# Kernel tuning notes

Measured on AMD Instinct MI355X. Metric: run time of the kernel, lower is better.

## Reference

```python
import jax, jax.numpy as jnp
import numpy as np

B, S, D, N = 16, 1024, 512, 2048
SPECTRAL_RADIUS = 0.95
SPARSITY = 0.01  # effective_sparsity = max(0.01, 5/N) = 0.01 for N=2048


def setup_inputs() -> dict:
    key = jax.random.key(0)
    k_x, k_fb, k_wraw, k_mask, k_win, k_wfb = jax.random.split(key, 6)
    x_seq = jax.random.normal(k_x, (B, S, D), dtype=jnp.float32)
    feedback_seq = jax.random.normal(k_fb, (B, S, D), dtype=jnp.float32)
    initial_state = jnp.zeros((B, N), dtype=jnp.float32)
    # Fixed random reservoir: sparse gaussian rescaled to spectral radius ~0.95.
    # For an NxN gaussian with density p, spectral radius ~= sqrt(N*p), so we
    # rescale by SPECTRAL_RADIUS / sqrt(N*p) (the torch code uses the exact
    # max eigenvalue; this approximation preserves the same math structure).
    W_raw = jax.random.normal(k_wraw, (N, N), dtype=jnp.float32)
    mask = (jax.random.uniform(k_mask, (N, N)) < SPARSITY).astype(jnp.float32)
    W_res = W_raw * mask * (SPECTRAL_RADIUS / jnp.sqrt(N * SPARSITY))
    W_in = jax.random.normal(k_win, (N, D), dtype=jnp.float32) * 0.1
    W_fb = jax.random.normal(k_wfb, (N, D), dtype=jnp.float32) * 0.1
    return {
        "x_seq": x_seq,
        "feedback_seq": feedback_seq,
        "initial_state": initial_state,
        "W_res": W_res,
        "W_in": W_in,
        "W_fb": W_fb,
    }


def reference(x_seq, feedback_seq, initial_state, W_res, W_in, W_fb):
    # Precompute input + feedback projections as one batched GEMM each
    # (same math as per-step einsums: 'bi,ni->bn' == x @ W.T).
    drive = jnp.einsum("bsd,nd->sbn", x_seq, W_in) + jnp.einsum(
        "bsd,nd->sbn", feedback_seq, W_fb
    )  # (S, B, N)

    def step(state, drive_t):
        # pre = state @ W_res.T + W_in x_t + W_fb fb_t
        new_state = jnp.tanh(state @ W_res.T + drive_t)
        return new_state, new_state

    _, states = jax.lax.scan(step, initial_state, drive)  # (S, B, N)
    return jnp.transpose(states, (1, 0, 2))  # (B, S, N)
```

## Files before the change

### kernel.cpp

```cpp
#include <hip/hip_runtime.h>
#include <stdint.h>

typedef unsigned short u16;
typedef unsigned int   u32;
typedef __attribute__((ext_vector_type(8))) short short8;
typedef __attribute__((ext_vector_type(4))) float f32x4;

#define CAP   52

__device__ __forceinline__ u16 rne_bf16(float f){
  u32 u = __float_as_uint(f);
  u32 r = (u + 0x7fffu + ((u >> 16) & 1u)) >> 16;
  return (u16)r;
}
__device__ __forceinline__ float bf16_to_f(u16 h){
  return __uint_as_float(((u32)h) << 16);
}
__device__ __forceinline__ float tanh_fast(float x){
  float e = __expf(2.0f * x);
  return 1.0f - 2.0f / (e + 1.0f);
}

__global__ __launch_bounds__(256) void pack_a_k(const float* __restrict__ x,
                                                const float* __restrict__ fb,
                                                u16* __restrict__ A){
  int idx = blockIdx.x * 256 + threadIdx.x;
  int m = idx >> 9, d = idx & 511;
  float xv = x[idx];
  float fv = fb[idx];
  u16 xh = rne_bf16(xv); u16 xl = rne_bf16(xv - bf16_to_f(xh));
  u16 fh = rne_bf16(fv); u16 fl = rne_bf16(fv - bf16_to_f(fh));
  size_t base = (size_t)m * 2048;
  A[base + d]        = xh;
  A[base + 512 + d]  = fh;
  A[base + 1024 + d] = xl;
  A[base + 1536 + d] = fl;
}

__global__ __launch_bounds__(256) void pack_b_k(const float* __restrict__ Win,
                                                const float* __restrict__ Wfb,
                                                const int* __restrict__ rowperm,
                                                u16* __restrict__ Bm){
  int idx = blockIdx.x * 256 + threadIdx.x;
  int n = idx >> 9, d = idx & 511;
  int row = rowperm[n];
  float iv = Win[(size_t)row * 512 + d];
  float fv = Wfb[(size_t)row * 512 + d];
  u16 ih = rne_bf16(iv); u16 il = rne_bf16(iv - bf16_to_f(ih));
  u16 fh = rne_bf16(fv); u16 fl = rne_bf16(fv - bf16_to_f(fh));
  size_t base = (size_t)n * 3072;
  Bm[base + d]        = ih;
  Bm[base + 512 + d]  = fh;
  Bm[base + 1024 + d] = ih;
  Bm[base + 1536 + d] = fh;
  Bm[base + 2048 + d] = il;
  Bm[base + 2560 + d] = fl;
}

#define GLDS(gp, lp) __builtin_amdgcn_global_load_lds( \
    (const __attribute__((address_space(1))) void*)(gp), \
    (__attribute__((address_space(3))) void*)(lp), 16, 0, 0)

__global__ __launch_bounds__(256) void gemm_k(const u16* __restrict__ A,
                                              const u16* __restrict__ Bm,
                                              float* __restrict__ C){
  __shared__ __align__(16) u16 As[128 * 32];
  __shared__ __align__(16) u16 Bs[128 * 32];
  const int tid = threadIdx.x;
  const int w = tid >> 6, l = tid & 63;
  const int bid = blockIdx.x;
  const int mt = bid >> 4, nt = bid & 15;
  const int m0 = mt * 128, n0 = nt * 128;
  const int srow = tid >> 2;
  const int scol = (tid & 3) * 8;
  const int wr = w & 1, wc = w >> 1;
  const int lhi = l >> 4, llo = l & 15;

  f32x4 acc[4][4];
  #pragma unroll
  for (int i = 0; i < 4; i++)
    #pragma unroll
    for (int j = 0; j < 4; j++)
      acc[i][j] = (f32x4){0.f, 0.f, 0.f, 0.f};

  for (int kt = 0; kt < 96; ++kt){
    int k = kt * 32;
    int keff = (k >= 2048) ? (k - 2048) : k;
    #pragma unroll
    for (int r = 0; r < 2; r++){
      const u16* ga = A  + (size_t)(m0 + r * 64 + srow) * 2048 + keff + scol;
      GLDS(ga, &As[r * 2048 + w * 512]);
      const u16* gb = Bm + (size_t)(n0 + r * 64 + srow) * 3072 + k + scol;
      GLDS(gb, &Bs[r * 2048 + w * 512]);
    }
    __syncthreads();
    short8 af[4], bf[4];
    #pragma unroll
    for (int i = 0; i < 4; i++){
      af[i] = *(const short8*)&As[(wr * 64 + i * 16 + llo) * 32 + lhi * 8];
      bf[i] = *(const short8*)&Bs[(wc * 64 + i * 16 + llo) * 32 + lhi * 8];
    }
    #pragma unroll
    for (int i = 0; i < 4; i++)
      #pragma unroll
      for (int j = 0; j < 4; j++)
        acc[i][j] = __builtin_amdgcn_mfma_f32_16x16x32_bf16(af[i], bf[j], acc[i][j], 0, 0, 0);
    __syncthreads();
  }
  #pragma unroll
  for (int i = 0; i < 4; i++)
    #pragma unroll
    for (int j = 0; j < 4; j++)
      #pragma unroll
      for (int rg = 0; rg < 4; rg++){
        int mr = m0 + wr * 64 + i * 16 + lhi * 4 + rg;
        int nc = n0 + wc * 64 + j * 16 + llo;
        C[(size_t)mr * 2048 + nc] = acc[i][j][rg];
      }
}

__global__ __launch_bounds__(256) void count_k(const float* __restrict__ W,
                                               int* __restrict__ nnz){
  int gt = blockIdx.x * 256 + threadIdx.x;
  int row = gt >> 6, l = gt & 63;
  const float* wr = W + (size_t)row * 2048;
  int c = 0;
  for (int i = 0; i < 32; i++) c += (wr[i * 64 + l] != 0.0f) ? 1 : 0;
  for (int off = 32; off; off >>= 1) c += __shfl_down(c, off, 64);
  if (l == 0) nnz[row] = c;
}

__global__ __launch_bounds__(1024) void sort_k(const int* __restrict__ nnz,
                                               u32* __restrict__ rowsp,
                                               int* __restrict__ L1a,
                                               int* __restrict__ rowperm){
  __shared__ int hist[64], off[64], cur[64];
  __shared__ int order[2048];
  int tid = threadIdx.x;
  if (tid < 64){ hist[tid] = 0; cur[tid] = 0; }
  __syncthreads();
  for (int r = tid; r < 2048; r += 1024){
    int b = nnz[r]; if (b > 63) b = 63;
    atomicAdd(&hist[b], 1);
  }
  __syncthreads();
  if (tid == 0){
    int run = 0;
    for (int b = 63; b >= 0; b--){ off[b] = run; run += hist[b]; }
  }
  __syncthreads();
  for (int r = tid; r < 2048; r += 1024){
    int b = nnz[r]; if (b > 63) b = 63;
    int pos = off[b] + atomicAdd(&cur[b], 1);
    order[pos] = r;
  }
  __syncthreads();
  int rA = order[tid], rB = order[2047 - tid];
  rowsp[tid] = (u32)rA | ((u32)rB << 16);
  L1a[tid] = nnz[rA];
  rowperm[tid] = rA;
  rowperm[tid + 1024] = rB;
}

__global__ __launch_bounds__(256) void fill_k(const float* __restrict__ W,
                                              const u32* __restrict__ rowsp,
                                              u32* __restrict__ wpk){
  int gt = blockIdx.x * 256 + threadIdx.x;
  int p = gt >> 6, l = gt & 63;
  u32 rp = rowsp[p];
  int rA = (int)(rp & 0xffffu), rB = (int)(rp >> 16);
  int base = 0;
  for (int h = 0; h < 2; h++){
    int row = h ? rB : rA;
    const float* wr = W + (size_t)row * 2048;
    int cnt = 0;
    for (int i = 0; i < 32; i++){
      int c = i * 64 + l;
      float v = wr[c];
      unsigned long long m = __ballot(v != 0.0f);
      int pre = __popcll(m & ((1ull << l) - 1ull));
      if (v != 0.0f){
        int s = base + cnt + pre;
        if (s < CAP){
          u32 addr = (u32)c << 2;
          u32 u = __float_as_uint(v);
          u = ((u - addr + 0x1000u) & 0xFFFFE000u) + addr;
          wpk[s * 1024 + p] = u;
        }
      }
      cnt += __popcll(m);
    }
    base += cnt;
  }
  for (int s = base + l; s < CAP; s += 64)
    wpk[s * 1024 + p] = 0u;
}

__global__ __launch_bounds__(64) void sched_k(u32* wpk,
                                              const u32* __restrict__ rowsp,
                                              const int* __restrict__ nnz){
  __shared__ u32 itm[64 * CAP];
  __shared__ int cnt[32];
  const int lane = threadIdx.x;
  const int p = blockIdx.x * 64 + lane;
  u32 rp = rowsp[p];
  int rA = (int)(rp & 0xffffu), rB = (int)(rp >> 16);
  int L1 = nnz[rA]; if (L1 > CAP) L1 = CAP;
  int nT = L1 + nnz[rB]; if (nT > CAP) nT = CAP;
  for (int k = 0; k < CAP; k++) itm[lane * CAP + k] = wpk[k * 1024 + p];
  __syncthreads();
  unsigned long long used = 0ull;
  for (int s = 0; s < CAP; s++){
    if (lane < 32) cnt[lane] = 0;
    __syncthreads();
    u32 word;
    if (s < nT){
      int lo = (s < L1) ? 0 : L1;
      int hi = (s < L1) ? L1 : nT;
      int chosen = -1;
      for (int capc = 2; chosen < 0; capc++){
        for (int j = lo; j < hi; j++){
          if (used & (1ull << j)) continue;
          u32 w = itm[lane * CAP + j];
          int bk = (int)((w >> 2) & 31u);
          int old = atomicAdd(&cnt[bk], 1);
          if (old < capc){ chosen = j; break; }
          atomicSub(&cnt[bk], 1);
        }
      }
      used |= 1ull << chosen;
      word = itm[lane * CAP + chosen];
    } else {
      int bsel = -1;
      for (int capc = 2; bsel < 0; capc++){
        for (int bk = 0; bk < 32; bk++){
          int old = atomicAdd(&cnt[bk], 1);
          if (old < capc){ bsel = bk; break; }
          atomicSub(&cnt[bk], 1);
        }
      }
      word = (u32)bsel << 2;
    }
    __syncthreads();
    wpk[s * 1024 + p] = word;
  }
}

__global__ __attribute__((amdgpu_flat_work_group_size(1024, 1024),
                          amdgpu_waves_per_eu(4, 4)))
void rnn_k(float* __restrict__ out,
           const float* __restrict__ init,
           const u32* __restrict__ wpkg,
           const u32* __restrict__ rowsp,
           const int* __restrict__ L1a){
  const int tid = threadIdx.x, b = blockIdx.x;
  u32 wk[CAP];
  #pragma unroll
  for (int k = 0; k < CAP; k++) wk[k] = wpkg[k * 1024 + tid];
  u32 rp = rowsp[tid];
  int rA = (int)(rp & 0xffffu), rB = (int)(rp >> 16);
  int L1 = L1a[tid];

  __shared__ float st[2048];
  st[tid]        = init[(size_t)b * 2048 + tid];
  st[tid + 1024] = init[(size_t)b * 2048 + tid + 1024];
  __syncthreads();
  const char* stb = (const char*)st;

  float* ob = out + (size_t)b * 1024 * 2048;
  float dA = __builtin_nontemporal_load(&ob[tid]);
  float dB = __builtin_nontemporal_load(&ob[tid + 1024]);
  for (int t = 0; t < 1024; t++){
    float* orow = ob + (size_t)t * 2048;
    const float* nrow = ob + (size_t)((t + 1) & 1023) * 2048;
    float dA2 = __builtin_nontemporal_load(&nrow[tid]);
    float dB2 = __builtin_nontemporal_load(&nrow[tid + 1024]);
    float aAll = 0.f, aA = 0.f;
    #pragma unroll
    for (int k = 0; k < CAP; k++){
      u32 w = wk[k];
      float sv = *(const float*)(stb + (w & 0x1FFCu));
      float pv = __uint_as_float(w) * sv;
      aAll += pv;
      aA += (k < L1) ? pv : 0.0f;
    }
    float preA = aA + dA;
    float preB = (aAll - aA) + dB;
    __syncthreads();
    float sA = tanh_fast(preA);
    float sB = tanh_fast(preB);
    st[rA] = sA; st[rB] = sB;
    __syncthreads();
    __builtin_nontemporal_store(st[tid], &orow[tid]);
    __builtin_nontemporal_store(st[tid + 1024], &orow[tid + 1024]);
    dA = dA2; dB = dB2;
  }
}

extern "C" void kernel_launch(void* const* d_in, const int* in_sizes, int n_in,
                              void* d_out, int out_size, void* d_ws, size_t ws_size,
                              hipStream_t stream) {
  const float* x    = (const float*)d_in[0];
  const float* fb   = (const float*)d_in[1];
  const float* init = (const float*)d_in[2];
  const float* Wres = (const float*)d_in[3];
  const float* Win  = (const float*)d_in[4];
  const float* Wfb  = (const float*)d_in[5];
  float* out = (float*)d_out;

  char* w8 = (char*)d_ws;
  u16*  A_pack = (u16*)(w8);
  u16*  B_pack = (u16*)(w8 + 67108864);
  u32*  wpk    = (u32*) (w8 + 79691776);
  int*  nnz    = (int*) (w8 + 79904768);
  u32*  rowsp  = (u32*) (w8 + 79912960);
  int*  L1a    = (int*) (w8 + 79917056);
  int*  rowperm= (int*) (w8 + 79921152);

  pack_a_k<<<32768, 256, 0, stream>>>(x, fb, A_pack);
  count_k<<<512, 256, 0, stream>>>(Wres, nnz);
  sort_k<<<1, 1024, 0, stream>>>(nnz, rowsp, L1a, rowperm);
  pack_b_k<<<4096, 256, 0, stream>>>(Win, Wfb, rowperm, B_pack);
  fill_k<<<256, 256, 0, stream>>>(Wres, rowsp, wpk);
  sched_k<<<16, 64, 0, stream>>>(wpk, rowsp, nnz);
  gemm_k<<<2048, 256, 0, stream>>>(A_pack, B_pack, out);
  rnn_k<<<16, 1024, 0, stream>>>(out, init, wpk, rowsp, L1a);
}
```

Baseline: 3.162 ms.

## Add iterative swap sweeps to reduce LDS bank conflicts in reservoir weight schedule

```diff
diff --git a/kernel.cpp b/kernel.cpp
--- a/kernel.cpp
+++ b/kernel.cpp
@@ -7,6 +7,7 @@
 typedef __attribute__((ext_vector_type(4))) float f32x4;
 
 #define CAP   52
+#define NSWEEP 48
 
 __device__ __forceinline__ u16 rne_bf16(float f){
   u32 u = __float_as_uint(f);
@@ -199,20 +200,23 @@
 __global__ __launch_bounds__(64) void sched_k(u32* wpk,
                                               const u32* __restrict__ rowsp,
                                               const int* __restrict__ nnz){
-  __shared__ u32 itm[64 * CAP];
-  __shared__ int cnt[32];
+  __shared__ u32 pool[CAP * 64];
+  __shared__ u32 itm[CAP * 64];
+  __shared__ int cnt[CAP * 32];
   const int lane = threadIdx.x;
   const int p = blockIdx.x * 64 + lane;
   u32 rp = rowsp[p];
   int rA = (int)(rp & 0xffffu), rB = (int)(rp >> 16);
   int L1 = nnz[rA]; if (L1 > CAP) L1 = CAP;
   int nT = L1 + nnz[rB]; if (nT > CAP) nT = CAP;
-  for (int k = 0; k < CAP; k++) itm[lane * CAP + k] = wpk[k * 1024 + p];
-  __syncthreads();
+
+  for (int i = lane; i < CAP * 32; i += 64) cnt[i] = 0;
+  for (int k = 0; k < CAP; k++) pool[k * 64 + lane] = wpk[k * 1024 + p];
+  __builtin_amdgcn_s_waitcnt(0);
+
   unsigned long long used = 0ull;
   for (int s = 0; s < CAP; s++){
-    if (lane < 32) cnt[lane] = 0;
-    __syncthreads();
+    int* c = &cnt[s * 32];
     u32 word;
     if (s < nT){
       int lo = (s < L1) ? 0 : L1;
@@ -221,29 +225,85 @@
       for (int capc = 2; chosen < 0; capc++){
         for (int j = lo; j < hi; j++){
           if (used & (1ull << j)) continue;
-          u32 w = itm[lane * CAP + j];
+          u32 w = pool[j * 64 + lane];
           int bk = (int)((w >> 2) & 31u);
-          int old = atomicAdd(&cnt[bk], 1);
+          int old = atomicAdd(&c[bk], 1);
           if (old < capc){ chosen = j; break; }
-          atomicSub(&cnt[bk], 1);
+          atomicSub(&c[bk], 1);
         }
       }
       used |= 1ull << chosen;
-      word = itm[lane * CAP + chosen];
+      word = pool[chosen * 64 + lane];
     } else {
       int bsel = -1;
       for (int capc = 2; bsel < 0; capc++){
-        for (int bk = 0; bk < 32; bk++){
-          int old = atomicAdd(&cnt[bk], 1);
+        for (int bk0 = 0; bk0 < 32; bk0++){
+          int bk = (bk0 + lane) & 31;
+          int old = atomicAdd(&c[bk], 1);
           if (old < capc){ bsel = bk; break; }
-          atomicSub(&cnt[bk], 1);
+          atomicSub(&c[bk], 1);
         }
       }
       word = (u32)bsel << 2;
     }
-    __syncthreads();
-    wpk[s * 1024 + p] = word;
-  }
+    itm[s * 64 + lane] = word;
+  }
+
+  for (int sweep = 0; sweep < NSWEEP; sweep++){
+    int fixes = 0;
+    for (int s1 = 0; s1 < CAP; s1++){
+      u32 w1 = itm[s1 * 64 + lane];
+      int b1 = (int)((w1 >> 2) & 31u);
+      if (cnt[s1 * 32 + b1] <= 2) continue;
+      if (s1 >= nT){
+        for (int bk0 = 1; bk0 < 32; bk0++){
+          int b2 = (b1 + bk0 + lane) & 31;
+          int old = atomicAdd(&cnt[s1 * 32 + b2], 1);
+          if (old < 2){
+            atomicSub(&cnt[s1 * 32 + b1], 1);
+            itm[s1 * 64 + lane] = (u32)b2 << 2;
+            fixes++; break;
+          }
+          atomicSub(&cnt[s1 * 32 + b2], 1);
+        }
+        continue;
+      }
+      int lo = (s1 < L1) ? 0 : L1;
+      int hi = (s1 < L1) ? L1 : nT;
+      int len = hi - lo;
+      if (len < 2) continue;
+      for (int d = 1; d < len; d++){
+        int s2 = lo + ((s1 - lo) + d + lane + sweep * 7) % len;
+        if (s2 == s1) continue;
+        u32 w2 = itm[s2 * 64 + lane];
+        int b2 = (int)((w2 >> 2) & 31u);
+        if (b1 == b2) continue;
+        if (cnt[s2 * 32 + b1] >= 2) continue;
+        if (cnt[s1 * 32 + b2] >= 2) continue;
+        int a = atomicSub(&cnt[s1 * 32 + b1], 1);
+        if (a <= 2){ atomicAdd(&cnt[s1 * 32 + b1], 1); break; }
+        int c2 = atomicAdd(&cnt[s1 * 32 + b2], 1);
+        if (c2 >= 2){
+          atomicSub(&cnt[s1 * 32 + b2], 1);
+          atomicAdd(&cnt[s1 * 32 + b1], 1); continue;
+        }
+        int c3 = atomicAdd(&cnt[s2 * 32 + b1], 1);
+        if (c3 >= 2){
+          atomicSub(&cnt[s2 * 32 + b1], 1);
+          atomicSub(&cnt[s1 * 32 + b2], 1);
+          atomicAdd(&cnt[s1 * 32 + b1], 1); continue;
+        }
+        atomicSub(&cnt[s2 * 32 + b2], 1);
+        itm[s1 * 64 + lane] = w2;
+        itm[s2 * 64 + lane] = w1;
+        fixes++; break;
+      }
+    }
+    if (__ballot(fixes != 0) == 0ull) break;
+  }
+
+  for (int s = 0; s < CAP; s++)
+    wpk[s * 1024 + p] = itm[s * 64 + lane];
 }
 
 __global__ __attribute__((amdgpu_flat_work_group_size(1024, 1024),
```

Result: slower. 3.985 ms (+26.0%).

## Double-buffer reservoir state and duplicate rotated copies to cut barriers and bank conflicts

Applied to the files above, without the earlier changes.

```diff
diff --git a/kernel.cpp b/kernel.cpp
--- a/kernel.cpp
+++ b/kernel.cpp
@@ -7,6 +7,7 @@
 typedef __attribute__((ext_vector_type(4))) float f32x4;
 
 #define CAP   52
+#define ROT   7
 
 __device__ __forceinline__ u16 rne_bf16(float f){
   u32 u = __float_as_uint(f);
@@ -164,7 +165,7 @@
 
 __global__ __launch_bounds__(256) void fill_k(const float* __restrict__ W,
                                               const u32* __restrict__ rowsp,
-                                              u32* __restrict__ wpk){
+                                              u32* __restrict__ raw){
   int gt = blockIdx.x * 256 + threadIdx.x;
   int p = gt >> 6, l = gt & 63;
   u32 rp = rowsp[p];
@@ -182,24 +183,22 @@
       if (v != 0.0f){
         int s = base + cnt + pre;
         if (s < CAP){
-          u32 addr = (u32)c << 2;
           u32 u = __float_as_uint(v);
-          u = ((u - addr + 0x1000u) & 0xFFFFE000u) + addr;
-          wpk[s * 1024 + p] = u;
+          u = ((u + 0x1000u) & 0xFFFFE000u) | (u32)c;
+          raw[s * 1024 + p] = u;
         }
       }
       cnt += __popcll(m);
     }
     base += cnt;
   }
-  for (int s = base + l; s < CAP; s += 64)
-    wpk[s * 1024 + p] = 0u;
-}
-
-__global__ __launch_bounds__(64) void sched_k(u32* wpk,
+}
+
+__global__ __launch_bounds__(64) void sched_k(const u32* __restrict__ raw,
+                                              u32* __restrict__ wpk,
                                               const u32* __restrict__ rowsp,
                                               const int* __restrict__ nnz){
-  __shared__ u32 itm[64 * CAP];
+  __shared__ u32 pool[CAP * 64];
   __shared__ int cnt[32];
   const int lane = threadIdx.x;
   const int p = blockIdx.x * 64 + lane;
@@ -207,12 +206,15 @@
   int rA = (int)(rp & 0xffffu), rB = (int)(rp >> 16);
   int L1 = nnz[rA]; if (L1 > CAP) L1 = CAP;
   int nT = L1 + nnz[rB]; if (nT > CAP) nT = CAP;
-  for (int k = 0; k < CAP; k++) itm[lane * CAP + k] = wpk[k * 1024 + p];
-  __syncthreads();
+
+  for (int k = 0; k < CAP; k++) pool[k * 64 + lane] = raw[k * 1024 + p];
+  __syncthreads();
+
   unsigned long long used = 0ull;
   for (int s = 0; s < CAP; s++){
     if (lane < 32) cnt[lane] = 0;
     __syncthreads();
+    const int par = s & 1;
     u32 word;
     if (s < nT){
       int lo = (s < L1) ? 0 : L1;
@@ -221,19 +223,24 @@
       for (int capc = 2; chosen < 0; capc++){
         for (int j = lo; j < hi; j++){
           if (used & (1ull << j)) continue;
-          u32 w = itm[lane * CAP + j];
-          int bk = (int)((w >> 2) & 31u);
+          int c = (int)(pool[j * 64 + lane] & 0x7FFu);
+          int bk = (par ? (c + ROT) : c) & 31;
           int old = atomicAdd(&cnt[bk], 1);
           if (old < capc){ chosen = j; break; }
           atomicSub(&cnt[bk], 1);
         }
       }
       used |= 1ull << chosen;
-      word = itm[lane * CAP + chosen];
+      u32 r = pool[chosen * 64 + lane];
+      u32 vb = r & 0xFFFFE000u;
+      u32 c  = r & 0x7FFu;
+      u32 ad = (u32)((par ? ((c + ROT) & 2047) : (int)c) << 2);
+      word = ((vb - ad + 0x1000u) & 0xFFFFE000u) + ad;
     } else {
       int bsel = -1;
       for (int capc = 2; bsel < 0; capc++){
-        for (int bk = 0; bk < 32; bk++){
+        for (int bb = 0; bb < 32; bb++){
+          int bk = (bb + lane) & 31;
           int old = atomicAdd(&cnt[bk], 1);
           if (old < capc){ bsel = bk; break; }
           atomicSub(&cnt[bk], 1);
@@ -258,43 +265,62 @@
   #pragma unroll
   for (int k = 0; k < CAP; k++) wk[k] = wpkg[k * 1024 + tid];
   u32 rp = rowsp[tid];
-  int rA = (int)(rp & 0xffffu), rB = (int)(rp >> 16);
-  int L1 = L1a[tid];
-
-  __shared__ float st[2048];
-  st[tid]        = init[(size_t)b * 2048 + tid];
-  st[tid + 1024] = init[(size_t)b * 2048 + tid + 1024];
+  const int rA = (int)(rp & 0xffffu), rB = (int)(rp >> 16);
+  const int L1 = L1a[tid];
+  const int wA0 = rA << 2;
+  const int wA1 = (((rA + ROT) & 2047) << 2) + 8192;
+  const int wB0 = rB << 2;
+  const int wB1 = (((rB + ROT) & 2047) << 2) + 8192;
+
+  __shared__ float st[8192];
+  float i0 = init[(size_t)b * 2048 + tid];
+  float i1 = init[(size_t)b * 2048 + tid + 1024];
+  st[tid] = i0;
+  st[tid + 1024] = i1;
+  st[2048 + ((tid + ROT) & 2047)] = i0;
+  st[2048 + ((tid + 1024 + ROT) & 2047)] = i1;
   __syncthreads();
   const char* stb = (const char*)st;
+  char* stw = (char*)st;
+  const int t4a = tid << 2, t4b = (tid + 1024) << 2;
 
   float* ob = out + (size_t)b * 1024 * 2048;
   float dA = __builtin_nontemporal_load(&ob[tid]);
   float dB = __builtin_nontemporal_load(&ob[tid + 1024]);
-  for (int t = 0; t < 1024; t++){
-    float* orow = ob + (size_t)t * 2048;
-    const float* nrow = ob + (size_t)((t + 1) & 1023) * 2048;
-    float dA2 = __builtin_nontemporal_load(&nrow[tid]);
-    float dB2 = __builtin_nontemporal_load(&nrow[tid + 1024]);
-    float aAll = 0.f, aA = 0.f;
-    #pragma unroll
-    for (int k = 0; k < CAP; k++){
-      u32 w = wk[k];
-      float sv = *(const float*)(stb + (w & 0x1FFCu));
-      float pv = __uint_as_float(w) * sv;
-      aAll += pv;
-      aA += (k < L1) ? pv : 0.0f;
-    }
-    float preA = aA + dA;
-    float preB = (aAll - aA) + dB;
-    __syncthreads();
-    float sA = tanh_fast(preA);
-    float sB = tanh_fast(preB);
-    st[rA] = sA; st[rB] = sB;
-    __syncthreads();
-    __builtin_nontemporal_store(st[tid], &orow[tid]);
-    __builtin_nontemporal_store(st[tid + 1024], &orow[tid + 1024]);
-    dA = dA2; dB = dB2;
-  }
+
+#define ESN_STEP(T, RD, WR) { \
+    float* orow = ob + (size_t)(T) * 2048; \
+    const float* nrow = ob + (size_t)(((T) + 1) & 1023) * 2048; \
+    float dA2 = __builtin_nontemporal_load(&nrow[tid]); \
+    float dB2 = __builtin_nontemporal_load(&nrow[tid + 1024]); \
+    float aAll = 0.f, aA = 0.f; \
+    _Pragma("unroll") \
+    for (int k = 0; k < CAP; k++){ \
+      u32 w = wk[k]; \
+      float sv = *(const float*)(stb + (RD) + ((k & 1) ? 8192 : 0) + (w & 0x1FFCu)); \
+      float pv = __uint_as_float(w) * sv; \
+      aAll += pv; \
+      aA += (k < L1) ? pv : 0.0f; \
+    } \
+    float preA = aA + dA; \
+    float preB = (aAll - aA) + dB; \
+    float sA = tanh_fast(preA); \
+    float sB = tanh_fast(preB); \
+    *(float*)(stw + (WR) + wA0) = sA; \
+    *(float*)(stw + (WR) + wA1) = sA; \
+    *(float*)(stw + (WR) + wB0) = sB; \
+    *(float*)(stw + (WR) + wB1) = sB; \
+    __syncthreads(); \
+    __builtin_nontemporal_store(*(const float*)(stb + (WR) + t4a), &orow[tid]); \
+    __builtin_nontemporal_store(*(const float*)(stb + (WR) + t4b), &orow[tid + 1024]); \
+    dA = dA2; dB = dB2; \
+  }
+
+  for (int t = 0; t < 1024; t += 2){
+    ESN_STEP(t, 0, 16384)
+    ESN_STEP(t + 1, 16384, 0)
+  }
+#undef ESN_STEP
 }
 
 extern "C" void kernel_launch(void* const* d_in, const int* in_sizes, int n_in,
@@ -316,13 +342,14 @@
   u32*  rowsp  = (u32*) (w8 + 79912960);
   int*  L1a    = (int*) (w8 + 79917056);
   int*  rowperm= (int*) (w8 + 79921152);
+  u32*  raw    = (u32*) out;
 
   pack_a_k<<<32768, 256, 0, stream>>>(x, fb, A_pack);
   count_k<<<512, 256, 0, stream>>>(Wres, nnz);
   sort_k<<<1, 1024, 0, stream>>>(nnz, rowsp, L1a, rowperm);
   pack_b_k<<<4096, 256, 0, stream>>>(Win, Wfb, rowperm, B_pack);
-  fill_k<<<256, 256, 0, stream>>>(Wres, rowsp, wpk);
-  sched_k<<<16, 64, 0, stream>>>(wpk, rowsp, nnz);
+  fill_k<<<256, 256, 0, stream>>>(Wres, rowsp, raw);
+  sched_k<<<16, 64, 0, stream>>>(raw, wpk, rowsp, nnz);
   gemm_k<<<2048, 256, 0, stream>>>(A_pack, B_pack, out);
   rnn_k<<<16, 1024, 0, stream>>>(out, init, wpk, rowsp, L1a);
 }
```

After: 3.582 ms. +13.3%, slower.

## Split each batch recurrence across two workgroups with global flag handshake

Applied to the files above, without the earlier changes.

```diff
diff --git a/kernel.cpp b/kernel.cpp
--- a/kernel.cpp
+++ b/kernel.cpp
@@ -6,7 +6,7 @@
 typedef __attribute__((ext_vector_type(8))) short short8;
 typedef __attribute__((ext_vector_type(4))) float f32x4;
 
-#define CAP   52
+#define CAP   56
 
 __device__ __forceinline__ u16 rne_bf16(float f){
   u32 u = __float_as_uint(f);
@@ -133,38 +133,47 @@
 __global__ __launch_bounds__(1024) void sort_k(const int* __restrict__ nnz,
                                                u32* __restrict__ rowsp,
                                                int* __restrict__ L1a,
-                                               int* __restrict__ rowperm){
-  __shared__ int hist[64], off[64], cur[64];
+                                               int* __restrict__ rowperm,
+                                               int* __restrict__ flags){
+  __shared__ int hist[128], off[128], cur[128];
   __shared__ int order[2048];
   int tid = threadIdx.x;
-  if (tid < 64){ hist[tid] = 0; cur[tid] = 0; }
-  __syncthreads();
-  for (int r = tid; r < 2048; r += 1024){
-    int b = nnz[r]; if (b > 63) b = 63;
-    atomicAdd(&hist[b], 1);
-  }
-  __syncthreads();
-  if (tid == 0){
+  if (tid < 32) flags[tid] = 0;
+  if (tid < 128){ hist[tid] = 0; cur[tid] = 0; }
+  __syncthreads();
+  {
+    int b0 = nnz[tid]; if (b0 > 63) b0 = 63;
+    atomicAdd(&hist[b0], 1);
+    int b1 = nnz[tid + 1024]; if (b1 > 63) b1 = 63;
+    atomicAdd(&hist[64 + b1], 1);
+  }
+  __syncthreads();
+  if (tid < 2){
     int run = 0;
-    for (int b = 63; b >= 0; b--){ off[b] = run; run += hist[b]; }
-  }
-  __syncthreads();
-  for (int r = tid; r < 2048; r += 1024){
-    int b = nnz[r]; if (b > 63) b = 63;
-    int pos = off[b] + atomicAdd(&cur[b], 1);
-    order[pos] = r;
-  }
-  __syncthreads();
-  int rA = order[tid], rB = order[2047 - tid];
+    for (int b = 63; b >= 0; b--){ off[tid * 64 + b] = run; run += hist[tid * 64 + b]; }
+  }
+  __syncthreads();
+  {
+    int b0 = nnz[tid]; if (b0 > 63) b0 = 63;
+    int pos = off[b0] + atomicAdd(&cur[b0], 1);
+    order[pos] = tid;
+    int b1 = nnz[tid + 1024]; if (b1 > 63) b1 = 63;
+    int pos1 = off[64 + b1] + atomicAdd(&cur[64 + b1], 1);
+    order[1024 + pos1] = tid + 1024;
+  }
+  __syncthreads();
+  int hh = tid >> 9, ii = tid & 511;
+  int rA = order[hh * 1024 + ii];
+  int rB = order[hh * 1024 + 1023 - ii];
   rowsp[tid] = (u32)rA | ((u32)rB << 16);
   L1a[tid] = nnz[rA];
-  rowperm[tid] = rA;
-  rowperm[tid + 1024] = rB;
+  rowperm[hh * 1024 + ii] = rA;
+  rowperm[hh * 1024 + 512 + ii] = rB;
 }
 
 __global__ __launch_bounds__(256) void fill_k(const float* __restrict__ W,
                                               const u32* __restrict__ rowsp,
-                                              u32* __restrict__ wpk){
+                                              u32* __restrict__ raw){
   int gt = blockIdx.x * 256 + threadIdx.x;
   int p = gt >> 6, l = gt & 63;
   u32 rp = rowsp[p];
@@ -182,24 +191,22 @@
       if (v != 0.0f){
         int s = base + cnt + pre;
         if (s < CAP){
-          u32 addr = (u32)c << 2;
           u32 u = __float_as_uint(v);
-          u = ((u - addr + 0x1000u) & 0xFFFFE000u) + addr;
-          wpk[s * 1024 + p] = u;
+          u = ((u + 0x1000u) & 0xFFFFE000u) | (u32)c;
+          raw[s * 1024 + p] = u;
         }
       }
       cnt += __popcll(m);
     }
     base += cnt;
   }
-  for (int s = base + l; s < CAP; s += 64)
-    wpk[s * 1024 + p] = 0u;
-}
-
-__global__ __launch_bounds__(64) void sched_k(u32* wpk,
+}
+
+__global__ __launch_bounds__(64) void sched_k(const u32* __restrict__ raw,
+                                              u32* __restrict__ wpk,
                                               const u32* __restrict__ rowsp,
                                               const int* __restrict__ nnz){
-  __shared__ u32 itm[64 * CAP];
+  __shared__ u32 pool[CAP * 64];
   __shared__ int cnt[32];
   const int lane = threadIdx.x;
   const int p = blockIdx.x * 64 + lane;
@@ -207,7 +214,7 @@
   int rA = (int)(rp & 0xffffu), rB = (int)(rp >> 16);
   int L1 = nnz[rA]; if (L1 > CAP) L1 = CAP;
   int nT = L1 + nnz[rB]; if (nT > CAP) nT = CAP;
-  for (int k = 0; k < CAP; k++) itm[lane * CAP + k] = wpk[k * 1024 + p];
+  for (int k = 0; k < CAP; k++) pool[k * 64 + lane] = raw[k * 1024 + p];
   __syncthreads();
   unsigned long long used = 0ull;
   for (int s = 0; s < CAP; s++){
@@ -221,19 +228,22 @@
       for (int capc = 2; chosen < 0; capc++){
         for (int j = lo; j < hi; j++){
           if (used & (1ull << j)) continue;
-          u32 w = itm[lane * CAP + j];
-          int bk = (int)((w >> 2) & 31u);
+          int bk = (int)(pool[j * 64 + lane] & 31u);
           int old = atomicAdd(&cnt[bk], 1);
           if (old < capc){ chosen = j; break; }
           atomicSub(&cnt[bk], 1);
         }
       }
       used |= 1ull << chosen;
-      word = itm[lane * CAP + chosen];
+      u32 r = pool[chosen * 64 + lane];
+      u32 vb = r & 0xFFFFE000u;
+      u32 ad = (r & 0x7FFu) << 2;
+      word = ((vb - ad + 0x1000u) & 0xFFFFE000u) + ad;
     } else {
       int bsel = -1;
       for (int capc = 2; bsel < 0; capc++){
-        for (int bk = 0; bk < 32; bk++){
+        for (int bb = 0; bb < 32; bb++){
+          int bk = (bb + lane) & 31;
           int old = atomicAdd(&cnt[bk], 1);
           if (old < capc){ bsel = bk; break; }
           atomicSub(&cnt[bk], 1);
@@ -246,35 +256,44 @@
   }
 }
 
-__global__ __attribute__((amdgpu_flat_work_group_size(1024, 1024),
-                          amdgpu_waves_per_eu(4, 4)))
+__global__ __attribute__((amdgpu_flat_work_group_size(512, 512),
+                          amdgpu_waves_per_eu(2, 2)))
 void rnn_k(float* __restrict__ out,
            const float* __restrict__ init,
            const u32* __restrict__ wpkg,
            const u32* __restrict__ rowsp,
-           const int* __restrict__ L1a){
-  const int tid = threadIdx.x, b = blockIdx.x;
+           const int* __restrict__ L1a,
+           int* flags){
+  const int tid = threadIdx.x;
+  const int b = blockIdx.x & 15, h = blockIdx.x >> 4;
+  const int q = h * 512 + tid;
   u32 wk[CAP];
   #pragma unroll
-  for (int k = 0; k < CAP; k++) wk[k] = wpkg[k * 1024 + tid];
-  u32 rp = rowsp[tid];
-  int rA = (int)(rp & 0xffffu), rB = (int)(rp >> 16);
-  int L1 = L1a[tid];
+  for (int k = 0; k < CAP; k++) wk[k] = wpkg[k * 1024 + q];
+  u32 rp = rowsp[q];
+  const int rA = (int)(rp & 0xffffu), rB = (int)(rp >> 16);
+  const int L1 = L1a[q];
+  const int own0 = h << 10, peer0 = (1 - h) << 10;
 
   __shared__ float st[2048];
-  st[tid]        = init[(size_t)b * 2048 + tid];
-  st[tid + 1024] = init[(size_t)b * 2048 + tid + 1024];
+  #pragma unroll
+  for (int j = 0; j < 4; j++)
+    st[j * 512 + tid] = init[(size_t)b * 2048 + j * 512 + tid];
   __syncthreads();
   const char* stb = (const char*)st;
 
   float* ob = out + (size_t)b * 1024 * 2048;
-  float dA = __builtin_nontemporal_load(&ob[tid]);
-  float dB = __builtin_nontemporal_load(&ob[tid + 1024]);
+  int* myf = &flags[h * 16 + b];
+  int* pf  = &flags[(1 - h) * 16 + b];
+
+  float dA = __builtin_nontemporal_load(&ob[own0 + tid]);
+  float dB = __builtin_nontemporal_load(&ob[own0 + 512 + tid]);
+
   for (int t = 0; t < 1024; t++){
-    float* orow = ob + (size_t)t * 2048;
+    float* row = ob + (size_t)t * 2048;
     const float* nrow = ob + (size_t)((t + 1) & 1023) * 2048;
-    float dA2 = __builtin_nontemporal_load(&nrow[tid]);
-    float dB2 = __builtin_nontemporal_load(&nrow[tid + 1024]);
+    float dA2 = __builtin_nontemporal_load(&nrow[own0 + tid]);
+    float dB2 = __builtin_nontemporal_load(&nrow[own0 + 512 + tid]);
     float aAll = 0.f, aA = 0.f;
     #pragma unroll
     for (int k = 0; k < CAP; k++){
@@ -284,15 +303,24 @@
       aAll += pv;
       aA += (k < L1) ? pv : 0.0f;
     }
-    float preA = aA + dA;
-    float preB = (aAll - aA) + dB;
-    __syncthreads();
-    float sA = tanh_fast(preA);
-    float sB = tanh_fast(preB);
+    float sA = tanh_fast(aA + dA);
+    float sB = tanh_fast((aAll - aA) + dB);
+    __builtin_nontemporal_store(sA, &row[rA]);
+    __builtin_nontemporal_store(sB, &row[rB]);
+    __syncthreads();
     st[rA] = sA; st[rB] = sB;
-    __syncthreads();
-    __builtin_nontemporal_store(st[tid], &orow[tid]);
-    __builtin_nontemporal_store(st[tid + 1024], &orow[tid + 1024]);
+    asm volatile("s_waitcnt vmcnt(0)" ::: "memory");
+    if (tid == 0){
+      __hip_atomic_store(myf, t + 1, __ATOMIC_RELAXED, __HIP_MEMORY_SCOPE_AGENT);
+      while (__hip_atomic_load(pf, __ATOMIC_ACQUIRE, __HIP_MEMORY_SCOPE_AGENT) <= t)
+        __builtin_amdgcn_s_sleep(1);
+    }
+    __syncthreads();
+    float p0 = __builtin_nontemporal_load(&row[peer0 + tid]);
+    float p1 = __builtin_nontemporal_load(&row[peer0 + 512 + tid]);
+    st[peer0 + tid] = p0;
+    st[peer0 + 512 + tid] = p1;
+    __syncthreads();
     dA = dA2; dB = dB2;
   }
 }
@@ -312,17 +340,19 @@
   u16*  A_pack = (u16*)(w8);
   u16*  B_pack = (u16*)(w8 + 67108864);
   u32*  wpk    = (u32*) (w8 + 79691776);
-  int*  nnz    = (int*) (w8 + 79904768);
-  u32*  rowsp  = (u32*) (w8 + 79912960);
-  int*  L1a    = (int*) (w8 + 79917056);
-  int*  rowperm= (int*) (w8 + 79921152);
+  int*  nnz    = (int*) (w8 + 79921152);
+  u32*  rowsp  = (u32*) (w8 + 79929344);
+  int*  L1a    = (int*) (w8 + 79933440);
+  int*  rowperm= (int*) (w8 + 79937536);
+  int*  flags  = (int*) (w8 + 79945728);
+  u32*  raw    = (u32*) out;
 
   pack_a_k<<<32768, 256, 0, stream>>>(x, fb, A_pack);
   count_k<<<512, 256, 0, stream>>>(Wres, nnz);
-  sort_k<<<1, 1024, 0, stream>>>(nnz, rowsp, L1a, rowperm);
+  sort_k<<<1, 1024, 0, stream>>>(nnz, rowsp, L1a, rowperm, flags);
   pack_b_k<<<4096, 256, 0, stream>>>(Win, Wfb, rowperm, B_pack);
-  fill_k<<<256, 256, 0, stream>>>(Wres, rowsp, wpk);
-  sched_k<<<16, 64, 0, stream>>>(wpk, rowsp, nnz);
+  fill_k<<<256, 256, 0, stream>>>(Wres, rowsp, raw);
+  sched_k<<<16, 64, 0, stream>>>(raw, wpk, rowsp, nnz);
   gemm_k<<<2048, 256, 0, stream>>>(A_pack, B_pack, out);
-  rnn_k<<<16, 1024, 0, stream>>>(out, init, wpk, rowsp, L1a);
-}
+  rnn_k<<<32, 512, 0, stream>>>(out, init, wpk, rowsp, L1a, flags);
+}
```

Measured after the change: 3.990 ms. +26.2%, slower.
